# Kernel tuning notes

Measured on AMD Instinct MI355X. Metric: run time of the kernel, lower is better.

The kernel has to match this reference:

```python
import jax, jax.numpy as jnp
import numpy as np

V, B, N, D, L, H = 30522, 32, 512, 512, 4, 8
HD = D // H
REC = L // 2  # block-recurrent layer index
SCALE = HD ** -0.5


def _ln(x, g, b):
    m = x.mean(-1, keepdims=True)
    v = ((x - m) ** 2).mean(-1, keepdims=True)
    return (x - m) / jnp.sqrt(v + 1e-5) * g + b


def _rope(t):
    # t: [b,h,n,hd]; rotary embedding on token positions (split-half convention)
    n = t.shape[2]
    inv = 1.0 / (10000.0 ** (jnp.arange(0, HD, 2, dtype=jnp.float32) / HD))
    f = jnp.arange(n, dtype=jnp.float32)[:, None] * inv  # [n, hd/2]
    cos, sin = jnp.cos(f), jnp.sin(f)
    t1, t2 = t[..., : HD // 2], t[..., HD // 2 :]
    return jnp.concatenate([t1 * cos - t2 * sin, t2 * cos + t1 * sin], -1)


def _heads(x):
    b, n, _ = x.shape
    return x.reshape(b, n, H, HD).transpose(0, 2, 1, 3)


def _merge(x):
    b, h, n, d = x.shape
    return x.transpose(0, 2, 1, 3).reshape(b, n, h * d)


def _attn(q, k, v, mask):
    s = jnp.einsum('bhid,bhjd->bhij', q, k) * SCALE
    if mask is not None:
        s = jnp.where(mask, s, jnp.float32(-1e9))
    a = jax.nn.softmax(s, axis=-1)
    return jnp.einsum('bhij,bhjd->bhid', a, v)


def setup_inputs() -> dict:
    key = jax.random.key(0)
    ks = jax.random.split(key, 12)
    w = lambda k, shp: jax.random.normal(k, shp, jnp.float32) * 0.02
    return {
        'ids': jax.random.randint(ks[0], (B, N), 0, V),
        'state': jax.random.normal(ks[1], (B, D), jnp.float32),
        'tok_emb': w(ks[2], (V, D)),
        'ln1_g': jnp.ones((L, D), jnp.float32), 'ln1_b': jnp.zeros((L, D), jnp.float32),
        'w_qkv': w(ks[3], (L, D, 3 * D)),
        'w_o': w(ks[4], (L, D, D)),
        'ln2_g': jnp.ones((L, D), jnp.float32), 'ln2_b': jnp.zeros((L, D), jnp.float32),
        'w_ff1': w(ks[5], (L, D, 4 * D)), 'b_ff1': jnp.zeros((L, 4 * D), jnp.float32),
        'w_ff2': w(ks[6], (L, 4 * D, D)), 'b_ff2': jnp.zeros((L, D), jnp.float32),
        's_ln_g': jnp.ones((D,), jnp.float32), 's_ln_b': jnp.zeros((D,), jnp.float32),
        'w_s_qkv': w(ks[7], (D, 3 * D)),
        'w_so': w(ks[8], (D, D)),
        'gate_beta': w(ks[9], (D,)),
        'f_ln_g': jnp.ones((D,), jnp.float32), 'f_ln_b': jnp.zeros((D,), jnp.float32),
        'head_w': w(ks[10], (D, 1)), 'head_b': jnp.zeros((1,), jnp.float32),
    }


def reference(ids, state, tok_emb, ln1_g, ln1_b, w_qkv, w_o, ln2_g, ln2_b,
              w_ff1, b_ff1, w_ff2, b_ff2, s_ln_g, s_ln_b, w_s_qkv, w_so,
              gate_beta, f_ln_g, f_ln_b, head_w, head_b):
    x = tok_emb[ids]                       # [b,n,d]
    s = state[:, None, :]                  # [b,1,d]  (state.unsqueeze(1))
    n = x.shape[1]
    causal = jnp.tril(jnp.ones((n, n), bool))
    for l in range(L):
        h = _ln(x, ln1_g[l], ln1_b[l])
        q, k, v = jnp.split(h @ w_qkv[l], 3, axis=-1)
        q, k, v = _heads(q), _heads(k), _heads(v)
        q, k = _rope(q), _rope(k)
        if l == REC:
            sn = _ln(s, s_ln_g, s_ln_b)
            sq, sk, sv = jnp.split(sn @ w_s_qkv, 3, axis=-1)
            sq, sk, sv = _heads(sq), _heads(sk), _heads(sv)
            # tokens attend over [tokens (causal), state vector (always visible)]
            m = jnp.concatenate([causal, jnp.ones((n, 1), bool)], axis=1)
            out_x = _attn(q, jnp.concatenate([k, sk], 2), jnp.concatenate([v, sv], 2), m)
            x = x + _merge(out_x) @ w_o[l]
            # state attends over [state, all tokens] (no mask)
            out_s = _attn(sq, jnp.concatenate([sk, k], 2), jnp.concatenate([sv, v], 2), None)
            upd = _merge(out_s) @ w_so
            g = jax.nn.sigmoid(gate_beta)   # fixed learned-EMA gate
            s = s * g + upd * (1.0 - g)
        else:
            out_x = _attn(q, k, v, causal)
            x = x + _merge(out_x) @ w_o[l]
        h2 = _ln(x, ln2_g[l], ln2_b[l])
        x = x + jax.nn.gelu(h2 @ w_ff1[l] + b_ff1[l]) @ w_ff2[l] + b_ff2[l]
    x = _ln(x, f_ln_g, f_ln_b)
    state_out = s[:, 0, :]                 # state[0].squeeze()
    logits = x @ head_w + head_b           # [b,n,1]
    out = jax.nn.log_softmax(logits, axis=-1)
    return out, state_out
```

## Files before the change

kernel.cpp:

```cpp
#include <hip/hip_runtime.h>
#include <hip/hip_bf16.h>
#include <math.h>

#define B_ 32
#define N_ 512
#define D_ 512
#define H_ 8
#define HD_ 64
#define QKV_ 1536
#define SCALE_ 0.125f

typedef unsigned short u16;
typedef unsigned int u32;
typedef __attribute__((ext_vector_type(8))) short bf16x8;
typedef __attribute__((ext_vector_type(4))) float f32x4;

#define GLOBAL_AS __attribute__((address_space(1)))
#define LDS_AS __attribute__((address_space(3)))

__device__ __forceinline__ float gelu_f(float x) {
  float u = 0.7978845608028654f * (x + 0.044715f * x * x * x);
  u = fminf(fmaxf(u, -15.f), 15.f);
  float e = __expf(2.f * u);
  float th = 1.f - 2.f * __builtin_amdgcn_rcpf(e + 1.f);
  return 0.5f * x * (1.0f + th);
}

__device__ __forceinline__ u16 f2b(float f) {
  union { float f; u32 u; } v;
  v.f = f;
  u32 r = (v.u + 0x7FFFu + ((v.u >> 16) & 1u)) >> 16;
  return (u16)r;
}

__device__ __forceinline__ float b2f(u16 x) {
  union { u32 u; float f; } v;
  v.u = ((u32)x) << 16;
  return v.f;
}

__device__ __forceinline__ int xcd_swz(int orig, int nwg) {
  int q = nwg >> 3, r = nwg & 7;
  int xcd = orig & 7, idx = orig >> 3;
  return (xcd < r ? xcd * (q + 1) : r * (q + 1) + (xcd - r) * q) + idx;
}

__global__ void k_prep(const float* __restrict__ w_qkv, const float* __restrict__ w_o,
                       const float* __restrict__ w_ff1, const float* __restrict__ w_ff2,
                       u16* __restrict__ wq_t, u16* __restrict__ wo_t,
                       u16* __restrict__ wf1_t, u16* __restrict__ wf2_t,
                       float* __restrict__ out0, float2* __restrict__ tab) {
  __shared__ float tile[32][33];
  int bid = blockIdx.x;
  int t = threadIdx.x;
  if (bid < 64) {
    int idx = bid * 256 + t;
    out0[idx] = 0.f;
    int n = idx >> 5, i = idx & 31;
    float inv = powf(10000.0f, -(float)i * (1.0f / 32.0f));
    float f = (float)n * inv;
    float s, c;
    sincosf(f, &s, &c);
    tab[idx] = make_float2(c, s);
    return;
  }
  int b2 = bid - 64;
  const float* W;
  u16* Wt;
  int K, N;
  if (b2 < 2304) {
    int l = b2 / 768; b2 -= l * 768;
    W = w_qkv + (size_t)l * D_ * QKV_; Wt = wq_t + (size_t)l * QKV_ * D_;
    K = D_; N = QKV_;
  } else if (b2 < 2816) {
    b2 -= 2304; int l = b2 >> 8; b2 &= 255;
    W = w_o + (size_t)l * D_ * D_; Wt = wo_t + (size_t)l * D_ * D_;
    K = D_; N = D_;
  } else if (b2 < 4864) {
    b2 -= 2816; int l = b2 >> 10; b2 &= 1023;
    W = w_ff1 + (size_t)l * D_ * 4 * D_; Wt = wf1_t + (size_t)l * 4 * D_ * D_;
    K = D_; N = 4 * D_;
  } else {
    b2 -= 4864; int l = b2 >> 10; b2 &= 1023;
    W = w_ff2 + (size_t)l * 4 * D_ * D_; Wt = wf2_t + (size_t)l * D_ * 4 * D_;
    K = 4 * D_; N = D_;
  }
  int nbx = N >> 5;
  int bx = b2 % nbx, by = b2 / nbx;
  int k0 = by * 32, n0 = bx * 32;
  int r = t >> 3, c4 = (t & 7) * 4;
  float4 v = *(const float4*)&W[(size_t)(k0 + r) * N + n0 + c4];
  tile[r][c4] = v.x; tile[r][c4 + 1] = v.y; tile[r][c4 + 2] = v.z; tile[r][c4 + 3] = v.w;
  __syncthreads();
  ushort4 o;
  o.x = f2b(tile[c4 + 0][r]); o.y = f2b(tile[c4 + 1][r]);
  o.z = f2b(tile[c4 + 2][r]); o.w = f2b(tile[c4 + 3][r]);
  *(ushort4*)&Wt[(size_t)(n0 + r) * K + k0 + c4] = o;
}

__global__ void k_embed(const int* __restrict__ ids, const float* __restrict__ emb,
                        float* __restrict__ x) {
  int row = blockIdx.x;
  int id = ids[row];
  const float4* s = (const float4*)(emb + (size_t)id * D_);
  float4* d = (float4*)(x + (size_t)row * D_);
  d[threadIdx.x] = s[threadIdx.x];
}

template <int BF16OUT>
__global__ void k_ln(const float* __restrict__ in, const float* __restrict__ gw,
                     const float* __restrict__ bw, void* __restrict__ outv) {
  int row = blockIdx.x * 4 + (threadIdx.x >> 6);
  int lane = threadIdx.x & 63;
  const float* p = in + (size_t)row * D_ + lane * 8;
  float4 v0 = *(const float4*)p;
  float4 v1 = *(const float4*)(p + 4);
  float s = v0.x + v0.y + v0.z + v0.w + v1.x + v1.y + v1.z + v1.w;
  float q = v0.x * v0.x + v0.y * v0.y + v0.z * v0.z + v0.w * v0.w +
            v1.x * v1.x + v1.y * v1.y + v1.z * v1.z + v1.w * v1.w;
#pragma unroll
  for (int o = 32; o >= 1; o >>= 1) {
    s += __shfl_xor(s, o);
    q += __shfl_xor(q, o);
  }
  float mean = s * (1.0f / D_);
  float var = q * (1.0f / D_) - mean * mean;
  float rstd = rsqrtf(var + 1e-5f);
  float4 g0 = *(const float4*)(gw + lane * 8);
  float4 g1 = *(const float4*)(gw + lane * 8 + 4);
  float4 b0 = *(const float4*)(bw + lane * 8);
  float4 b1 = *(const float4*)(bw + lane * 8 + 4);
  float o8[8];
  o8[0] = (v0.x - mean) * rstd * g0.x + b0.x;
  o8[1] = (v0.y - mean) * rstd * g0.y + b0.y;
  o8[2] = (v0.z - mean) * rstd * g0.z + b0.z;
  o8[3] = (v0.w - mean) * rstd * g0.w + b0.w;
  o8[4] = (v1.x - mean) * rstd * g1.x + b1.x;
  o8[5] = (v1.y - mean) * rstd * g1.y + b1.y;
  o8[6] = (v1.z - mean) * rstd * g1.z + b1.z;
  o8[7] = (v1.w - mean) * rstd * g1.w + b1.w;
  if (BF16OUT) {
    u16* op = (u16*)outv + (size_t)row * D_ + lane * 8;
    ushort4 a, b;
    a.x = f2b(o8[0]); a.y = f2b(o8[1]); a.z = f2b(o8[2]); a.w = f2b(o8[3]);
    b.x = f2b(o8[4]); b.y = f2b(o8[5]); b.z = f2b(o8[6]); b.w = f2b(o8[7]);
    *(ushort4*)op = a;
    *(ushort4*)(op + 4) = b;
  } else {
    float* op = (float*)outv + (size_t)row * D_ + lane * 8;
    *(float4*)op = make_float4(o8[0], o8[1], o8[2], o8[3]);
    *(float4*)(op + 4) = make_float4(o8[4], o8[5], o8[6], o8[7]);
  }
}

template <int EPI, int BF16OUT>
__global__ __launch_bounds__(256) void k_mgemm(
    const u16* __restrict__ A, const u16* __restrict__ Bt,
    const float* __restrict__ bias, const float* __restrict__ resid,
    void* __restrict__ Cv, int M, int K, int Nc, int nb0) {
  __shared__ u16 As[2][2][128 * 32];
  __shared__ u16 Bs[2][2][128 * 32];
  int t = threadIdx.x;
  int wave = t >> 6, lane = t & 63;
  int nwg = gridDim.x * gridDim.y;
  int swz = xcd_swz(blockIdx.y * gridDim.x + blockIdx.x, nwg);
  int m0 = (swz / gridDim.x) * 128;
  int n0 = ((swz % gridDim.x) + nb0) * 128;
  int wr = wave >> 1, wc = wave & 1;
  f32x4 acc[4][4] = {};

  int srow = lane >> 2;
  int scol = ((lane & 3) ^ ((lane >> 3) & 3)) * 8;
  const u16* gaBase = A + (size_t)(m0 + wave * 32 + srow) * K + scol;
  const u16* gbBase = Bt + (size_t)(n0 + wave * 32 + srow) * K + scol;

#define STAGE_MG(bsel, sub, kk)                                                \
  {                                                                            \
    _Pragma("unroll") for (int i_ = 0; i_ < 2; ++i_) {                         \
      int rbase_ = wave * 32 + i_ * 16;                                        \
      __builtin_amdgcn_global_load_lds(                                        \
          (const GLOBAL_AS void*)(gaBase + (size_t)(i_ * 16) * K + (kk)),      \
          (LDS_AS void*)&As[bsel][sub][rbase_ * 32], 16, 0, 0);                \
      __builtin_amdgcn_global_load_lds(                                        \
          (const GLOBAL_AS void*)(gbBase + (size_t)(i_ * 16) * K + (kk)),      \
          (LDS_AS void*)&Bs[bsel][sub][rbase_ * 32], 16, 0, 0);                \
    }                                                                          \
  }

  int c = lane & 15, g = lane >> 4;
  int chread = (g ^ ((c >> 1) & 3)) * 8;

  int nIter = K >> 6;
  STAGE_MG(0, 0, 0);
  STAGE_MG(0, 1, 32);
  __syncthreads();
  for (int it = 0; it < nIter; ++it) {
    int cur = it & 1;
    if (it + 1 < nIter) {
      STAGE_MG(cur ^ 1, 0, (size_t)(it + 1) * 64);
      STAGE_MG(cur ^ 1, 1, (size_t)(it + 1) * 64 + 32);
    }
#pragma unroll
    for (int sub = 0; sub < 2; ++sub) {
      const u16* as = As[cur][sub];
      const u16* bs = Bs[cur][sub];
      bf16x8 af[4], bfr[4];
#pragma unroll
      for (int mi = 0; mi < 4; ++mi)
        af[mi] = *(const bf16x8*)&as[(wr * 64 + mi * 16 + c) * 32 + chread];
#pragma unroll
      for (int ni = 0; ni < 4; ++ni)
        bfr[ni] = *(const bf16x8*)&bs[(wc * 64 + ni * 16 + c) * 32 + chread];
#pragma unroll
      for (int mi = 0; mi < 4; ++mi)
#pragma unroll
        for (int ni = 0; ni < 4; ++ni)
          acc[mi][ni] = __builtin_amdgcn_mfma_f32_16x16x32_bf16(bfr[ni], af[mi], acc[mi][ni], 0, 0, 0);
    }
    __syncthreads();
  }
#undef STAGE_MG

#pragma unroll
  for (int mi = 0; mi < 4; ++mi) {
    int m = m0 + wr * 64 + mi * 16 + (lane & 15);
    size_t rowoff = (size_t)m * Nc;
#pragma unroll
    for (int ni = 0; ni < 4; ++ni) {
      int n = n0 + wc * 64 + ni * 16 + (lane >> 4) * 4;
      float v0 = acc[mi][ni][0], v1 = acc[mi][ni][1],
            v2 = acc[mi][ni][2], v3 = acc[mi][ni][3];
      if (EPI == 2 || EPI == 3) {
        float4 bb = *(const float4*)&bias[n];
        v0 += bb.x; v1 += bb.y; v2 += bb.z; v3 += bb.w;
      }
      if (EPI == 2) {
        v0 = gelu_f(v0); v1 = gelu_f(v1); v2 = gelu_f(v2); v3 = gelu_f(v3);
      }
      if (EPI == 1 || EPI == 3) {
        float4 rr = *(const float4*)&resid[rowoff + n];
        v0 += rr.x; v1 += rr.y; v2 += rr.z; v3 += rr.w;
      }
      if (BF16OUT) {
        ushort4 o;
        o.x = f2b(v0); o.y = f2b(v1); o.z = f2b(v2); o.w = f2b(v3);
        *(ushort4*)&((u16*)Cv)[rowoff + n] = o;
      } else {
        *(float4*)&((float*)Cv)[rowoff + n] = make_float4(v0, v1, v2, v3);
      }
    }
  }
}

template <int EPI>
__global__ __launch_bounds__(256) void k_gemm(const float* __restrict__ A,
                                              const float* __restrict__ W,
                                              const float* __restrict__ bias,
                                              const float* __restrict__ resid,
                                              float* __restrict__ C,
                                              int M, int K, int Nc) {
  __shared__ float As[32][68];
  __shared__ float Bs[32][68];
  int t = threadIdx.x;
  int tx = t & 15, ty = t >> 4;
  int m0 = blockIdx.y * 64, n0 = blockIdx.x * 64;
  float acc[4][4] = {};
  int ar = t >> 2, akc = (t & 3) * 8;
  int bkr = t >> 3, bnc = (t & 7) * 8;
  int garow = m0 + ar;
  bool aval = garow < M;
  const float* Aptr = A + (size_t)(aval ? garow : 0) * K + akc;
  const float* Wptr = W + (size_t)bkr * Nc + n0 + bnc;

  for (int k0 = 0; k0 < K; k0 += 32) {
    float4 a0, a1;
    if (aval) {
      a0 = *(const float4*)(Aptr + k0);
      a1 = *(const float4*)(Aptr + k0 + 4);
    } else {
      a0 = make_float4(0.f, 0.f, 0.f, 0.f);
      a1 = a0;
    }
    As[akc + 0][ar] = a0.x; As[akc + 1][ar] = a0.y;
    As[akc + 2][ar] = a0.z; As[akc + 3][ar] = a0.w;
    As[akc + 4][ar] = a1.x; As[akc + 5][ar] = a1.y;
    As[akc + 6][ar] = a1.z; As[akc + 7][ar] = a1.w;
    float4 b0 = *(const float4*)(Wptr + (size_t)k0 * Nc);
    float4 b1 = *(const float4*)(Wptr + (size_t)k0 * Nc + 4);
    *(float4*)&Bs[bkr][bnc] = b0;
    *(float4*)&Bs[bkr][bnc + 4] = b1;
    __syncthreads();
#pragma unroll
    for (int k = 0; k < 32; ++k) {
      float4 av = *(float4*)&As[k][ty * 4];
      float4 bv = *(float4*)&Bs[k][tx * 4];
      float a[4] = {av.x, av.y, av.z, av.w};
      float b[4] = {bv.x, bv.y, bv.z, bv.w};
#pragma unroll
      for (int i = 0; i < 4; ++i)
#pragma unroll
        for (int j = 0; j < 4; ++j) acc[i][j] += a[i] * b[j];
    }
    __syncthreads();
  }
#pragma unroll
  for (int i = 0; i < 4; ++i) {
    int m = m0 + ty * 4 + i;
    if (m >= M) break;
    size_t off = (size_t)m * Nc + n0 + tx * 4;
    float r[4];
#pragma unroll
    for (int j = 0; j < 4; ++j) {
      float v = acc[i][j];
      if (EPI == 2 || EPI == 3) v += bias[n0 + tx * 4 + j];
      if (EPI == 2) v = gelu_f(v);
      if (EPI == 1 || EPI == 3) v += resid[off + j];
      r[j] = v;
    }
    *(float4*)&C[off] = make_float4(r[0], r[1], r[2], r[3]);
  }
}

__global__ __launch_bounds__(512) void k_fattn(const u16* __restrict__ qkv,
                                               const float2* __restrict__ tab,
                                               u16* __restrict__ out) {
  __shared__ u16 Kl[64 * 64];
  __shared__ u16 Vt[64 * 64];
  __shared__ u16 Pl[8][16 * 64];
  int swz = xcd_swz(blockIdx.x, gridDim.x);
  int p = swz & 1, h = (swz >> 1) & 7, b = swz >> 4;
  int qtA = p, qtB = 3 - p;
  int t = threadIdx.x;
  int w = t >> 6, lane = t & 63;
  int c = lane & 15, g = lane >> 4;

  auto loadQ = [&](int qt, bf16x8* qa) {
    int n = qt * 128 + w * 16 + c;
    const u16* qptr = qkv + (size_t)(b * N_ + n) * QKV_ + h * HD_ + g * 8;
    union { bf16x8 v; u16 s[8]; } a0, a1, r0, r1;
    a0.v = *(const bf16x8*)qptr;
    a1.v = *(const bf16x8*)(qptr + 32);
    const float2* tb = tab + n * 32 + g * 8;
#pragma unroll
    for (int j = 0; j < 8; ++j) {
      float2 cs = tb[j];
      float lo = b2f(a0.s[j]), hi = b2f(a1.s[j]);
      r0.s[j] = f2b((lo * cs.x - hi * cs.y) * SCALE_);
      r1.s[j] = f2b((hi * cs.x + lo * cs.y) * SCALE_);
    }
    qa[0] = r0.v;
    qa[1] = r1.v;
  };

  bf16x8 qaA[2], qaB[2];
  loadQ(qtA, qaA);
  loadQ(qtB, qaB);

  f32x4 OA[4] = {}, OB[4] = {};
  float mA[4], lA[4], mB[4], lB[4];
#pragma unroll
  for (int r = 0; r < 4; ++r) { mA[r] = mB[r] = -1e30f; lA[r] = lB[r] = 0.f; }

  int myA = 2 * qtA + (w >> 2), myB = 2 * qtB + (w >> 2);
  int ktmax = 2 * qtB + 1;

  union { bf16x8 v; u16 s[8]; } rk0, rk1;
  ushort4 rv0a, rv0b, rv1a, rv1b;
  int krow = t >> 2, ki0 = (t & 3) * 8;
  int tt = t - 256, vkp = (tt >> 3) * 2, vd0 = (tt & 7) * 8;

  auto loadT = [&](int kt) {
    if (t < 256) {
      const u16* base = qkv + (size_t)(b * N_ + kt * 64 + krow) * QKV_ + D_ + h * HD_;
      rk0.v = *(const bf16x8*)(base + ki0);
      rk1.v = *(const bf16x8*)(base + ki0 + 32);
    } else {
      const u16* v0p = qkv + (size_t)(b * N_ + kt * 64 + vkp) * QKV_ + 2 * D_ + h * HD_ + vd0;
      const u16* v1p = v0p + QKV_;
      rv0a = *(const ushort4*)v0p;
      rv0b = *(const ushort4*)(v0p + 4);
      rv1a = *(const ushort4*)v1p;
      rv1b = *(const ushort4*)(v1p + 4);
    }
  };

  auto writeT = [&](int kt) {
    if (t < 256) {
      int n = kt * 64 + krow;
      const float2* tb = tab + n * 32 + ki0;
      union { bf16x8 v; u16 s[8]; } olo, ohi;
#pragma unroll
      for (int j = 0; j < 8; ++j) {
        float2 cs = tb[j];
        float fl = b2f(rk0.s[j]), fh = b2f(rk1.s[j]);
        olo.s[j] = f2b(fl * cs.x - fh * cs.y);
        ohi.s[j] = f2b(fh * cs.x + fl * cs.y);
      }
      int bb = krow * 128 + ki0 * 2, sw = (krow & 7) << 4;
      *(bf16x8*)((char*)Kl + (bb ^ sw)) = olo.v;
      *(bf16x8*)((char*)Kl + ((bb + 64) ^ sw)) = ohi.v;
    } else {
      u16 a0[8] = {rv0a.x, rv0a.y, rv0a.z, rv0a.w, rv0b.x, rv0b.y, rv0b.z, rv0b.w};
      u16 a1[8] = {rv1a.x, rv1a.y, rv1a.z, rv1a.w, rv1b.x, rv1b.y, rv1b.z, rv1b.w};
      u32* VtW = (u32*)Vt;
#pragma unroll
      for (int j = 0; j < 8; ++j) {
        int d = vd0 + j;
        VtW[(d * 32 + (vkp >> 1)) ^ ((d & 7) << 2)] = ((u32)a1[j] << 16) | (u32)a0[j];
      }
    }
  };

  auto compute = [&](const bf16x8* qa, f32x4* O, float* m_r, float* l_r,
                     int myblk, int qt, int kt) {
    f32x4 s[4] = {};
#pragma unroll
    for (int ks = 0; ks < 2; ++ks) {
#pragma unroll
      for (int nt = 0; nt < 4; ++nt) {
        int kr = nt * 16 + c;
        int byteoff = (kr * 128 + (g * 8 + ks * 32) * 2) ^ ((kr & 7) << 4);
        bf16x8 kb = *(const bf16x8*)((const char*)Kl + byteoff);
        s[nt] = __builtin_amdgcn_mfma_f32_16x16x32_bf16(qa[ks], kb, s[nt], 0, 0, 0);
      }
    }
    if (kt == myblk) {
#pragma unroll
      for (int nt = 0; nt < 4; ++nt)
#pragma unroll
        for (int r = 0; r < 4; ++r)
          if (kt * 64 + nt * 16 + c > qt * 128 + w * 16 + g * 4 + r) s[nt][r] = -1e30f;
    }
    float tm[4], tl[4], fac[4];
#pragma unroll
    for (int r = 0; r < 4; ++r)
      tm[r] = fmaxf(fmaxf(s[0][r], s[1][r]), fmaxf(s[2][r], s[3][r]));
#pragma unroll
    for (int msk = 1; msk <= 8; msk <<= 1)
#pragma unroll
      for (int r = 0; r < 4; ++r)
        tm[r] = fmaxf(tm[r], __shfl_xor(tm[r], msk));
#pragma unroll
    for (int r = 0; r < 4; ++r) {
      float mn = fmaxf(m_r[r], tm[r]);
      fac[r] = __expf(m_r[r] - mn);
      m_r[r] = mn;
      tl[r] = 0.f;
    }
    u16* plw = Pl[w];
#pragma unroll
    for (int nt = 0; nt < 4; ++nt) {
#pragma unroll
      for (int r = 0; r < 4; ++r) {
        float pv = __expf(s[nt][r] - m_r[r]);
        tl[r] += pv;
        int q = g * 4 + r, kk = nt * 16 + c;
        plw[(q * 64 + kk) ^ ((q & 7) << 3)] = f2b(pv);
      }
    }
#pragma unroll
    for (int msk = 1; msk <= 8; msk <<= 1)
#pragma unroll
      for (int r = 0; r < 4; ++r) tl[r] += __shfl_xor(tl[r], msk);
#pragma unroll
    for (int r = 0; r < 4; ++r) l_r[r] = l_r[r] * fac[r] + tl[r];
#pragma unroll
    for (int nt = 0; nt < 4; ++nt)
#pragma unroll
      for (int r = 0; r < 4; ++r) O[nt][r] *= fac[r];
#pragma unroll
    for (int ks = 0; ks < 2; ++ks) {
      int pbyte = (c * 128 + (g * 8 + ks * 32) * 2) ^ ((c & 7) << 4);
      bf16x8 pa = *(const bf16x8*)((const char*)plw + pbyte);
#pragma unroll
      for (int nt = 0; nt < 4; ++nt) {
        int d = nt * 16 + c;
        int vbyte = (d * 128 + (g * 8 + ks * 32) * 2) ^ ((d & 7) << 4);
        bf16x8 vb = *(const bf16x8*)((const char*)Vt + vbyte);
        O[nt] = __builtin_amdgcn_mfma_f32_16x16x32_bf16(pa, vb, O[nt], 0, 0, 0);
      }
    }
  };

  loadT(0);
  for (int kt = 0; kt <= ktmax; ++kt) {
    writeT(kt);
    __syncthreads();
    if (kt < ktmax) loadT(kt + 1);
    if (kt <= myA) compute(qaA, OA, mA, lA, myA, qtA, kt);
    if (kt <= myB) compute(qaB, OB, mB, lB, myB, qtB, kt);
    __syncthreads();
  }

  auto store = [&](int qt, const f32x4* O, const float* l_r) {
    u16* dst = out + (size_t)(b * N_ + qt * 128 + w * 16) * D_ + h * HD_;
#pragma unroll
    for (int nt = 0; nt < 4; ++nt) {
#pragma unroll
      for (int r = 0; r < 4; ++r) {
        int q = g * 4 + r;
        dst[(size_t)q * D_ + nt * 16 + c] = f2b(O[nt][r] / l_r[r]);
      }
    }
  };
  store(qtA, OA, lA);
  store(qtB, OB, lB);
}

__global__ __launch_bounds__(128) void k_state_attn(const float* __restrict__ sqkv,
                                                    const u16* __restrict__ qkv,
                                                    const float2* __restrict__ tab,
                                                    float* __restrict__ outs) {
  int h = blockIdx.x, b = blockIdx.y;
  __shared__ float sq[HD_];
  __shared__ float sc[513];
  __shared__ float red[128];
  int t = threadIdx.x;
  if (t < HD_) sq[t] = sqkv[(size_t)b * QKV_ + h * HD_ + t];
  __syncthreads();
  for (int j = t; j < 513; j += 128) {
    float acc = 0.f;
    if (j == 0) {
      const float* kp = sqkv + (size_t)b * QKV_ + D_ + h * HD_;
#pragma unroll
      for (int d = 0; d < HD_; ++d) acc += sq[d] * kp[d];
    } else {
      const u16* kp = qkv + (size_t)(b * N_ + j - 1) * QKV_ + D_ + h * HD_;
      const float2* tb = tab + (size_t)(j - 1) * 32;
#pragma unroll
      for (int d = 0; d < 32; ++d) {
        float2 cs = tb[d];
        float klo = b2f(kp[d]), khi = b2f(kp[d + 32]);
        acc += sq[d] * (klo * cs.x - khi * cs.y) + sq[d + 32] * (khi * cs.x + klo * cs.y);
      }
    }
    sc[j] = acc * SCALE_;
  }
  __syncthreads();
  float m = -1e30f;
  for (int j = t; j < 513; j += 128) m = fmaxf(m, sc[j]);
  red[t] = m;
  __syncthreads();
  for (int s = 64; s > 0; s >>= 1) {
    if (t < s) red[t] = fmaxf(red[t], red[t + s]);
    __syncthreads();
  }
  m = red[0];
  __syncthreads();
  float sum = 0.f;
  for (int j = t; j < 513; j += 128) {
    float p = expf(sc[j] - m);
    sc[j] = p;
    sum += p;
  }
  red[t] = sum;
  __syncthreads();
  for (int s = 64; s > 0; s >>= 1) {
    if (t < s) red[t] += red[t + s];
    __syncthreads();
  }
  float tot = red[0];
  if (t < HD_) {
    int d = t;
    float acc = sc[0] * sqkv[(size_t)b * QKV_ + 2 * D_ + h * HD_ + d];
    for (int j = 1; j <= N_; ++j)
      acc += sc[j] * b2f(qkv[(size_t)(b * N_ + j - 1) * QKV_ + 2 * D_ + h * HD_ + d]);
    outs[(size_t)b * D_ + h * HD_ + d] = acc / tot;
  }
}

__global__ void k_gate(const float* __restrict__ state, const float* __restrict__ upd,
                       const float* __restrict__ beta, float* __restrict__ out2) {
  int idx = blockIdx.x * 256 + threadIdx.x;
  int c = idx & (D_ - 1);
  float g = __builtin_amdgcn_rcpf(1.0f + __expf(-beta[c]));
  out2[idx] = state[idx] * g + upd[idx] * (1.0f - g);
}

extern "C" void kernel_launch(void* const* d_in, const int* in_sizes, int n_in,
                              void* d_out, int out_size, void* d_ws, size_t ws_size,
                              hipStream_t stream) {
  (void)in_sizes; (void)n_in; (void)out_size; (void)ws_size;
  const int* ids = (const int*)d_in[0];
  const float* state = (const float*)d_in[1];
  const float* tok_emb = (const float*)d_in[2];
  const float* ln1_g = (const float*)d_in[3];
  const float* ln1_b = (const float*)d_in[4];
  const float* w_qkv = (const float*)d_in[5];
  const float* w_o = (const float*)d_in[6];
  const float* ln2_g = (const float*)d_in[7];
  const float* ln2_b = (const float*)d_in[8];
  const float* w_ff1 = (const float*)d_in[9];
  const float* b_ff1 = (const float*)d_in[10];
  const float* w_ff2 = (const float*)d_in[11];
  const float* b_ff2 = (const float*)d_in[12];
  const float* s_ln_g = (const float*)d_in[13];
  const float* s_ln_b = (const float*)d_in[14];
  const float* w_s_qkv = (const float*)d_in[15];
  const float* w_so = (const float*)d_in[16];
  const float* gate_beta = (const float*)d_in[17];

  float* out0 = (float*)d_out;
  float* out1 = (float*)d_out + 16384;

  float* ws = (float*)d_ws;
  float* x = ws;
  u16* qkv_bf = (u16*)(ws + 8388608);
  u16* mid_bf = qkv_bf;
  u16* h_bf = (u16*)(ws + 25165824);
  u16* ao_bf = (u16*)(ws + 29360128);
  u16* wq_t = (u16*)(ws + 33554432);
  u16* wo_t = (u16*)(ws + 34734080);
  u16* wf1_t = (u16*)(ws + 34996224);
  u16* wf2_t = (u16*)(ws + 36044800);
  float* sln = ws + 37093376;
  float* sqkv = sln + 16384;
  float* souts = sqkv + 49152;
  float* supd = souts + 16384;
  float2* tab = (float2*)(ws + 37191680);

  const int M = B_ * N_;

  k_prep<<<dim3(6976), dim3(256), 0, stream>>>(w_qkv, w_o, w_ff1, w_ff2,
                                               wq_t, wo_t, wf1_t, wf2_t, out0, tab);
  k_embed<<<dim3(M), dim3(128), 0, stream>>>(ids, tok_emb, x);

  for (int l = 0; l < 3; ++l) {
    k_ln<1><<<dim3(M / 4), dim3(256), 0, stream>>>(x, ln1_g + l * D_, ln1_b + l * D_, h_bf);
    if (l == 2) {
      k_mgemm<0, 1><<<dim3(8, 128), dim3(256), 0, stream>>>(
          h_bf, wq_t + (size_t)l * QKV_ * D_, nullptr, nullptr, qkv_bf, M, D_, QKV_, 4);
      break;
    }
    k_mgemm<0, 1><<<dim3(12, 128), dim3(256), 0, stream>>>(
        h_bf, wq_t + (size_t)l * QKV_ * D_, nullptr, nullptr, qkv_bf, M, D_, QKV_, 0);
    k_fattn<<<dim3(2 * H_ * B_), dim3(512), 0, stream>>>(qkv_bf, tab, ao_bf);
    k_mgemm<1, 0><<<dim3(4, 128), dim3(256), 0, stream>>>(
        ao_bf, wo_t + (size_t)l * D_ * D_, nullptr, x, x, M, D_, D_, 0);
    k_ln<1><<<dim3(M / 4), dim3(256), 0, stream>>>(x, ln2_g + l * D_, ln2_b + l * D_, h_bf);
    k_mgemm<2, 1><<<dim3(16, 128), dim3(256), 0, stream>>>(
        h_bf, wf1_t + (size_t)l * 4 * D_ * D_, b_ff1 + l * 4 * D_, nullptr, mid_bf, M, D_, 4 * D_, 0);
    k_mgemm<3, 0><<<dim3(4, 128), dim3(256), 0, stream>>>(
        mid_bf, wf2_t + (size_t)l * D_ * 4 * D_, b_ff2 + l * D_, x, x, M, 4 * D_, D_, 0);
  }

  k_ln<0><<<dim3(B_ / 4), dim3(256), 0, stream>>>(state, s_ln_g, s_ln_b, sln);
  k_gemm<0><<<dim3(24, 1), dim3(256), 0, stream>>>(
      sln, w_s_qkv, nullptr, nullptr, sqkv, B_, D_, QKV_);
  k_state_attn<<<dim3(H_, B_), dim3(128), 0, stream>>>(sqkv, qkv_bf, tab, souts);
  k_gemm<0><<<dim3(8, 1), dim3(256), 0, stream>>>(
      souts, w_so, nullptr, nullptr, supd, B_, D_, D_);
  k_gate<<<dim3(64), dim3(256), 0, stream>>>(state, supd, gate_beta, out1);
}
```

Measured before the change: 635.8 us.

## Store residual stream in bf16 and fuse state-path kernels into one

The residual stream x is now kept in bf16 instead of fp32. The embedding, layernorm and residual-add GEMM epilogues read and write half as many bytes, which cuts memory traffic on the bandwidth-bound LN and embed passes. Separately, the five small state-path launches (LN, QKV gemm, attention, output gemm, gate) are merged into one kernel per batch row, removing launch overhead and intermediate buffers. The trade-off is lower residual precision, which can build up rounding error across layers, and a state kernel that runs only 32 blocks.

Result: slower. 687.4 us (+8.1%).

```diff
diff --git a/kernel.cpp b/kernel.cpp
--- a/kernel.cpp
+++ b/kernel.cpp
@@ -99,25 +99,27 @@
 }
 
 __global__ void k_embed(const int* __restrict__ ids, const float* __restrict__ emb,
-                        float* __restrict__ x) {
+                        u16* __restrict__ x) {
   int row = blockIdx.x;
   int id = ids[row];
-  const float4* s = (const float4*)(emb + (size_t)id * D_);
-  float4* d = (float4*)(x + (size_t)row * D_);
-  d[threadIdx.x] = s[threadIdx.x];
-}
-
-template <int BF16OUT>
-__global__ void k_ln(const float* __restrict__ in, const float* __restrict__ gw,
-                     const float* __restrict__ bw, void* __restrict__ outv) {
+  float4 v = ((const float4*)(emb + (size_t)id * D_))[threadIdx.x];
+  ushort4 o;
+  o.x = f2b(v.x); o.y = f2b(v.y); o.z = f2b(v.z); o.w = f2b(v.w);
+  ((ushort4*)(x + (size_t)row * D_))[threadIdx.x] = o;
+}
+
+__global__ void k_ln(const u16* __restrict__ in, const float* __restrict__ gw,
+                     const float* __restrict__ bw, u16* __restrict__ out) {
   int row = blockIdx.x * 4 + (threadIdx.x >> 6);
   int lane = threadIdx.x & 63;
-  const float* p = in + (size_t)row * D_ + lane * 8;
-  float4 v0 = *(const float4*)p;
-  float4 v1 = *(const float4*)(p + 4);
-  float s = v0.x + v0.y + v0.z + v0.w + v1.x + v1.y + v1.z + v1.w;
-  float q = v0.x * v0.x + v0.y * v0.y + v0.z * v0.z + v0.w * v0.w +
-            v1.x * v1.x + v1.y * v1.y + v1.z * v1.z + v1.w * v1.w;
+  union { bf16x8 v; u16 s[8]; } u;
+  u.v = *(const bf16x8*)(in + (size_t)row * D_ + lane * 8);
+  float f[8];
+#pragma unroll
+  for (int j = 0; j < 8; ++j) f[j] = b2f(u.s[j]);
+  float s = 0.f, q = 0.f;
+#pragma unroll
+  for (int j = 0; j < 8; ++j) { s += f[j]; q += f[j] * f[j]; }
 #pragma unroll
   for (int o = 32; o >= 1; o >>= 1) {
     s += __shfl_xor(s, o);
@@ -130,33 +132,18 @@
   float4 g1 = *(const float4*)(gw + lane * 8 + 4);
   float4 b0 = *(const float4*)(bw + lane * 8);
   float4 b1 = *(const float4*)(bw + lane * 8 + 4);
-  float o8[8];
-  o8[0] = (v0.x - mean) * rstd * g0.x + b0.x;
-  o8[1] = (v0.y - mean) * rstd * g0.y + b0.y;
-  o8[2] = (v0.z - mean) * rstd * g0.z + b0.z;
-  o8[3] = (v0.w - mean) * rstd * g0.w + b0.w;
-  o8[4] = (v1.x - mean) * rstd * g1.x + b1.x;
-  o8[5] = (v1.y - mean) * rstd * g1.y + b1.y;
-  o8[6] = (v1.z - mean) * rstd * g1.z + b1.z;
-  o8[7] = (v1.w - mean) * rstd * g1.w + b1.w;
-  if (BF16OUT) {
-    u16* op = (u16*)outv + (size_t)row * D_ + lane * 8;
-    ushort4 a, b;
-    a.x = f2b(o8[0]); a.y = f2b(o8[1]); a.z = f2b(o8[2]); a.w = f2b(o8[3]);
-    b.x = f2b(o8[4]); b.y = f2b(o8[5]); b.z = f2b(o8[6]); b.w = f2b(o8[7]);
-    *(ushort4*)op = a;
-    *(ushort4*)(op + 4) = b;
-  } else {
-    float* op = (float*)outv + (size_t)row * D_ + lane * 8;
-    *(float4*)op = make_float4(o8[0], o8[1], o8[2], o8[3]);
-    *(float4*)(op + 4) = make_float4(o8[4], o8[5], o8[6], o8[7]);
-  }
+  float gg[8] = {g0.x, g0.y, g0.z, g0.w, g1.x, g1.y, g1.z, g1.w};
+  float bb[8] = {b0.x, b0.y, b0.z, b0.w, b1.x, b1.y, b1.z, b1.w};
+  union { bf16x8 v; u16 s[8]; } ov;
+#pragma unroll
+  for (int j = 0; j < 8; ++j) ov.s[j] = f2b((f[j] - mean) * rstd * gg[j] + bb[j]);
+  *(bf16x8*)(out + (size_t)row * D_ + lane * 8) = ov.v;
 }
 
 template <int EPI, int BF16OUT>
 __global__ __launch_bounds__(256) void k_mgemm(
     const u16* __restrict__ A, const u16* __restrict__ Bt,
-    const float* __restrict__ bias, const float* __restrict__ resid,
+    const float* __restrict__ bias, const u16* __restrict__ resid,
     void* __restrict__ Cv, int M, int K, int Nc, int nb0) {
   __shared__ u16 As[2][2][128 * 32];
   __shared__ u16 Bs[2][2][128 * 32];
@@ -238,8 +225,8 @@
         v0 = gelu_f(v0); v1 = gelu_f(v1); v2 = gelu_f(v2); v3 = gelu_f(v3);
       }
       if (EPI == 1 || EPI == 3) {
-        float4 rr = *(const float4*)&resid[rowoff + n];
-        v0 += rr.x; v1 += rr.y; v2 += rr.z; v3 += rr.w;
+        ushort4 rr = *(const ushort4*)&resid[rowoff + n];
+        v0 += b2f(rr.x); v1 += b2f(rr.y); v2 += b2f(rr.z); v3 += b2f(rr.w);
       }
       if (BF16OUT) {
         ushort4 o;
@@ -249,75 +236,6 @@
         *(float4*)&((float*)Cv)[rowoff + n] = make_float4(v0, v1, v2, v3);
       }
     }
-  }
-}
-
-template <int EPI>
-__global__ __launch_bounds__(256) void k_gemm(const float* __restrict__ A,
-                                              const float* __restrict__ W,
-                                              const float* __restrict__ bias,
-                                              const float* __restrict__ resid,
-                                              float* __restrict__ C,
-                                              int M, int K, int Nc) {
-  __shared__ float As[32][68];
-  __shared__ float Bs[32][68];
-  int t = threadIdx.x;
-  int tx = t & 15, ty = t >> 4;
-  int m0 = blockIdx.y * 64, n0 = blockIdx.x * 64;
-  float acc[4][4] = {};
-  int ar = t >> 2, akc = (t & 3) * 8;
-  int bkr = t >> 3, bnc = (t & 7) * 8;
-  int garow = m0 + ar;
-  bool aval = garow < M;
-  const float* Aptr = A + (size_t)(aval ? garow : 0) * K + akc;
-  const float* Wptr = W + (size_t)bkr * Nc + n0 + bnc;
-
-  for (int k0 = 0; k0 < K; k0 += 32) {
-    float4 a0, a1;
-    if (aval) {
-      a0 = *(const float4*)(Aptr + k0);
-      a1 = *(const float4*)(Aptr + k0 + 4);
-    } else {
-      a0 = make_float4(0.f, 0.f, 0.f, 0.f);
-      a1 = a0;
-    }
-    As[akc + 0][ar] = a0.x; As[akc + 1][ar] = a0.y;
-    As[akc + 2][ar] = a0.z; As[akc + 3][ar] = a0.w;
-    As[akc + 4][ar] = a1.x; As[akc + 5][ar] = a1.y;
-    As[akc + 6][ar] = a1.z; As[akc + 7][ar] = a1.w;
-    float4 b0 = *(const float4*)(Wptr + (size_t)k0 * Nc);
-    float4 b1 = *(const float4*)(Wptr + (size_t)k0 * Nc + 4);
-    *(float4*)&Bs[bkr][bnc] = b0;
-    *(float4*)&Bs[bkr][bnc + 4] = b1;
-    __syncthreads();
-#pragma unroll
-    for (int k = 0; k < 32; ++k) {
-      float4 av = *(float4*)&As[k][ty * 4];
-      float4 bv = *(float4*)&Bs[k][tx * 4];
-      float a[4] = {av.x, av.y, av.z, av.w};
-      float b[4] = {bv.x, bv.y, bv.z, bv.w};
-#pragma unroll
-      for (int i = 0; i < 4; ++i)
-#pragma unroll
-        for (int j = 0; j < 4; ++j) acc[i][j] += a[i] * b[j];
-    }
-    __syncthreads();
-  }
-#pragma unroll
-  for (int i = 0; i < 4; ++i) {
-    int m = m0 + ty * 4 + i;
-    if (m >= M) break;
-    size_t off = (size_t)m * Nc + n0 + tx * 4;
-    float r[4];
-#pragma unroll
-    for (int j = 0; j < 4; ++j) {
-      float v = acc[i][j];
-      if (EPI == 2 || EPI == 3) v += bias[n0 + tx * 4 + j];
-      if (EPI == 2) v = gelu_f(v);
-      if (EPI == 1 || EPI == 3) v += resid[off + j];
-      r[j] = v;
-    }
-    *(float4*)&C[off] = make_float4(r[0], r[1], r[2], r[3]);
   }
 }
 
@@ -507,74 +425,117 @@
   store(qtB, OB, lB);
 }
 
-__global__ __launch_bounds__(128) void k_state_attn(const float* __restrict__ sqkv,
-                                                    const u16* __restrict__ qkv,
-                                                    const float2* __restrict__ tab,
-                                                    float* __restrict__ outs) {
-  int h = blockIdx.x, b = blockIdx.y;
-  __shared__ float sq[HD_];
-  __shared__ float sc[513];
-  __shared__ float red[128];
+__global__ __launch_bounds__(256) void k_state(
+    const float* __restrict__ state, const float* __restrict__ g_ln,
+    const float* __restrict__ b_ln, const float* __restrict__ w_sqkv,
+    const float* __restrict__ w_so, const float* __restrict__ beta,
+    const u16* __restrict__ qkv, const float2* __restrict__ tab,
+    float* __restrict__ out2) {
+  int b = blockIdx.x;
   int t = threadIdx.x;
-  if (t < HD_) sq[t] = sqkv[(size_t)b * QKV_ + h * HD_ + t];
+  __shared__ float sln[512];
+  __shared__ float sq[1536];
+  __shared__ float sc[8][513];
+  __shared__ float souts[512];
+  __shared__ float wrs[4], wrq[4];
+
+  float v0 = state[b * D_ + 2 * t], v1 = state[b * D_ + 2 * t + 1];
+  float s = v0 + v1, q = v0 * v0 + v1 * v1;
+#pragma unroll
+  for (int o = 32; o >= 1; o >>= 1) { s += __shfl_xor(s, o); q += __shfl_xor(q, o); }
+  int w = t >> 6, lane = t & 63;
+  if (lane == 0) { wrs[w] = s; wrq[w] = q; }
   __syncthreads();
-  for (int j = t; j < 513; j += 128) {
-    float acc = 0.f;
-    if (j == 0) {
-      const float* kp = sqkv + (size_t)b * QKV_ + D_ + h * HD_;
-#pragma unroll
-      for (int d = 0; d < HD_; ++d) acc += sq[d] * kp[d];
-    } else {
-      const u16* kp = qkv + (size_t)(b * N_ + j - 1) * QKV_ + D_ + h * HD_;
-      const float2* tb = tab + (size_t)(j - 1) * 32;
-#pragma unroll
-      for (int d = 0; d < 32; ++d) {
-        float2 cs = tb[d];
-        float klo = b2f(kp[d]), khi = b2f(kp[d + 32]);
-        acc += sq[d] * (klo * cs.x - khi * cs.y) + sq[d + 32] * (khi * cs.x + klo * cs.y);
-      }
-    }
-    sc[j] = acc * SCALE_;
-  }
+  s = wrs[0] + wrs[1] + wrs[2] + wrs[3];
+  q = wrq[0] + wrq[1] + wrq[2] + wrq[3];
+  float mean = s * (1.0f / D_);
+  float var = q * (1.0f / D_) - mean * mean;
+  float rstd = rsqrtf(var + 1e-5f);
+  sln[2 * t] = (v0 - mean) * rstd * g_ln[2 * t] + b_ln[2 * t];
+  sln[2 * t + 1] = (v1 - mean) * rstd * g_ln[2 * t + 1] + b_ln[2 * t + 1];
   __syncthreads();
+
+  {
+    float acc[6] = {};
+#pragma unroll 4
+    for (int d = 0; d < 512; ++d) {
+      float sv = sln[d];
+      const float* wr = w_sqkv + (size_t)d * QKV_ + t;
+#pragma unroll
+      for (int p = 0; p < 6; ++p) acc[p] += sv * wr[p * 256];
+    }
+#pragma unroll
+    for (int p = 0; p < 6; ++p) sq[p * 256 + t] = acc[p];
+  }
+  __syncthreads();
+
+  int h = t >> 5, li = t & 31;
+  {
+    const float* sqq = sq + h * HD_;
+    for (int j = li; j < 513; j += 32) {
+      float acc = 0.f;
+      if (j == 0) {
+        const float* kp = sq + D_ + h * HD_;
+#pragma unroll
+        for (int d = 0; d < HD_; ++d) acc += sqq[d] * kp[d];
+      } else {
+        const u16* kp = qkv + (size_t)(b * N_ + j - 1) * QKV_ + D_ + h * HD_;
+        const float2* tb = tab + (size_t)(j - 1) * 32;
+#pragma unroll
+        for (int d = 0; d < 32; ++d) {
+          float2 cs = tb[d];
+          float klo = b2f(kp[d]), khi = b2f(kp[d + 32]);
+          acc += sqq[d] * (klo * cs.x - khi * cs.y) + sqq[d + 32] * (khi * cs.x + klo * cs.y);
+        }
+      }
+      sc[h][j] = acc * SCALE_;
+    }
+  }
   float m = -1e30f;
-  for (int j = t; j < 513; j += 128) m = fmaxf(m, sc[j]);
-  red[t] = m;
+  for (int j = li; j < 513; j += 32) m = fmaxf(m, sc[h][j]);
+#pragma unroll
+  for (int o = 16; o >= 1; o >>= 1) m = fmaxf(m, __shfl_xor(m, o));
+  float sum = 0.f;
+  for (int j = li; j < 513; j += 32) {
+    float p = __expf(sc[h][j] - m);
+    sc[h][j] = p;
+    sum += p;
+  }
+#pragma unroll
+  for (int o = 16; o >= 1; o >>= 1) sum += __shfl_xor(sum, o);
+  float inv = __builtin_amdgcn_rcpf(sum);
   __syncthreads();
-  for (int s = 64; s > 0; s >>= 1) {
-    if (t < s) red[t] = fmaxf(red[t], red[t + s]);
-    __syncthreads();
-  }
-  m = red[0];
+  {
+    int d0 = li * 2;
+    const float* svp = sq + 2 * D_ + h * HD_;
+    float a0 = sc[h][0] * svp[d0];
+    float a1 = sc[h][0] * svp[d0 + 1];
+    for (int j = 1; j <= N_; ++j) {
+      const u16* vp = qkv + (size_t)(b * N_ + j - 1) * QKV_ + 2 * D_ + h * HD_ + d0;
+      float p = sc[h][j];
+      a0 += p * b2f(vp[0]);
+      a1 += p * b2f(vp[1]);
+    }
+    souts[h * HD_ + d0] = a0 * inv;
+    souts[h * HD_ + d0 + 1] = a1 * inv;
+  }
   __syncthreads();
-  float sum = 0.f;
-  for (int j = t; j < 513; j += 128) {
-    float p = expf(sc[j] - m);
-    sc[j] = p;
-    sum += p;
-  }
-  red[t] = sum;
-  __syncthreads();
-  for (int s = 64; s > 0; s >>= 1) {
-    if (t < s) red[t] += red[t + s];
-    __syncthreads();
-  }
-  float tot = red[0];
-  if (t < HD_) {
-    int d = t;
-    float acc = sc[0] * sqkv[(size_t)b * QKV_ + 2 * D_ + h * HD_ + d];
-    for (int j = 1; j <= N_; ++j)
-      acc += sc[j] * b2f(qkv[(size_t)(b * N_ + j - 1) * QKV_ + 2 * D_ + h * HD_ + d]);
-    outs[(size_t)b * D_ + h * HD_ + d] = acc / tot;
-  }
-}
-
-__global__ void k_gate(const float* __restrict__ state, const float* __restrict__ upd,
-                       const float* __restrict__ beta, float* __restrict__ out2) {
-  int idx = blockIdx.x * 256 + threadIdx.x;
-  int c = idx & (D_ - 1);
-  float g = __builtin_amdgcn_rcpf(1.0f + __expf(-beta[c]));
-  out2[idx] = state[idx] * g + upd[idx] * (1.0f - g);
+
+  {
+    float acc0 = 0.f, acc1 = 0.f;
+#pragma unroll 4
+    for (int d = 0; d < 512; ++d) {
+      float sv = souts[d];
+      const float* wr = w_so + (size_t)d * D_ + t;
+      acc0 += sv * wr[0];
+      acc1 += sv * wr[256];
+    }
+    int c0 = t, c1 = t + 256;
+    float g0 = __builtin_amdgcn_rcpf(1.0f + __expf(-beta[c0]));
+    float g1 = __builtin_amdgcn_rcpf(1.0f + __expf(-beta[c1]));
+    out2[b * D_ + c0] = state[b * D_ + c0] * g0 + acc0 * (1.0f - g0);
+    out2[b * D_ + c1] = state[b * D_ + c1] * g1 + acc1 * (1.0f - g1);
+  }
 }
 
 extern "C" void kernel_launch(void* const* d_in, const int* in_sizes, int n_in,
@@ -604,7 +565,7 @@
   float* out1 = (float*)d_out + 16384;
 
   float* ws = (float*)d_ws;
-  float* x = ws;
+  u16* x = (u16*)ws;
   u16* qkv_bf = (u16*)(ws + 8388608);
   u16* mid_bf = qkv_bf;
   u16* h_bf = (u16*)(ws + 25165824);
@@ -613,10 +574,6 @@
   u16* wo_t = (u16*)(ws + 34734080);
   u16* wf1_t = (u16*)(ws + 34996224);
   u16* wf2_t = (u16*)(ws + 36044800);
-  float* sln = ws + 37093376;
-  float* sqkv = sln + 16384;
-  float* souts = sqkv + 49152;
-  float* supd = souts + 16384;
   float2* tab = (float2*)(ws + 37191680);
 
   const int M = B_ * N_;
@@ -626,7 +583,7 @@
   k_embed<<<dim3(M), dim3(128), 0, stream>>>(ids, tok_emb, x);
 
   for (int l = 0; l < 3; ++l) {
-    k_ln<1><<<dim3(M / 4), dim3(256), 0, stream>>>(x, ln1_g + l * D_, ln1_b + l * D_, h_bf);
+    k_ln<<<dim3(M / 4), dim3(256), 0, stream>>>(x, ln1_g + l * D_, ln1_b + l * D_, h_bf);
     if (l == 2) {
       k_mgemm<0, 1><<<dim3(8, 128), dim3(256), 0, stream>>>(
           h_bf, wq_t + (size_t)l * QKV_ * D_, nullptr, nullptr, qkv_bf, M, D_, QKV_, 4);
@@ -635,20 +592,15 @@
     k_mgemm<0, 1><<<dim3(12, 128), dim3(256), 0, stream>>>(
         h_bf, wq_t + (size_t)l * QKV_ * D_, nullptr, nullptr, qkv_bf, M, D_, QKV_, 0);
     k_fattn<<<dim3(2 * H_ * B_), dim3(512), 0, stream>>>(qkv_bf, tab, ao_bf);
-    k_mgemm<1, 0><<<dim3(4, 128), dim3(256), 0, stream>>>(
+    k_mgemm<1, 1><<<dim3(4, 128), dim3(256), 0, stream>>>(
         ao_bf, wo_t + (size_t)l * D_ * D_, nullptr, x, x, M, D_, D_, 0);
-    k_ln<1><<<dim3(M / 4), dim3(256), 0, stream>>>(x, ln2_g + l * D_, ln2_b + l * D_, h_bf);
+    k_ln<<<dim3(M / 4), dim3(256), 0, stream>>>(x, ln2_g + l * D_, ln2_b + l * D_, h_bf);
     k_mgemm<2, 1><<<dim3(16, 128), dim3(256), 0, stream>>>(
         h_bf, wf1_t + (size_t)l * 4 * D_ * D_, b_ff1 + l * 4 * D_, nullptr, mid_bf, M, D_, 4 * D_, 0);
-    k_mgemm<3, 0><<<dim3(4, 128), dim3(256), 0, stream>>>(
+    k_mgemm<3, 1><<<dim3(4, 128), dim3(256), 0, stream>>>(
         mid_bf, wf2_t + (size_t)l * D_ * 4 * D_, b_ff2 + l * D_, x, x, M, 4 * D_, D_, 0);
   }
 
-  k_ln<0><<<dim3(B_ / 4), dim3(256), 0, stream>>>(state, s_ln_g, s_ln_b, sln);
-  k_gemm<0><<<dim3(24, 1), dim3(256), 0, stream>>>(
-      sln, w_s_qkv, nullptr, nullptr, sqkv, B_, D_, QKV_);
-  k_state_attn<<<dim3(H_, B_), dim3(128), 0, stream>>>(sqkv, qkv_bf, tab, souts);
-  k_gemm<0><<<dim3(8, 1), dim3(256), 0, stream>>>(
-      souts, w_so, nullptr, nullptr, supd, B_, D_, D_);
-  k_gate<<<dim3(64), dim3(256), 0, stream>>>(state, supd, gate_beta, out1);
-}
+  k_state<<<dim3(B_), dim3(256), 0, stream>>>(state, s_ln_g, s_ln_b, w_s_qkv,
+                                              w_so, gate_beta, qkv_bf, tab, out1);
+}
```
